# Optimization experiments

Hardware: AMD Instinct MI355X
Metric: run time of the kernel (lower is better)

## Reference

```python
import jax, jax.numpy as jnp
import numpy as np

N_NODES = 50000
EPS = 1e-12  # F.normalize eps


def sage_conv(x, src, dst, W_l, b_l, W_r):
    # PyG SAGEConv: out = lin_l(mean_j x_j) + lin_r(x_i), then L2 normalize.
    n = x.shape[0]
    agg = jax.ops.segment_sum(x[src], dst, num_segments=n)          # [N, d]
    cnt = jax.ops.segment_sum(jnp.ones_like(src, dtype=x.dtype), dst,
                              num_segments=n)                       # [N]
    mean = agg / jnp.maximum(cnt, 1.0)[:, None]
    out = mean @ W_l.T + b_l + x @ W_r.T
    norm = jnp.linalg.norm(out, axis=-1, keepdims=True)
    return out / jnp.maximum(norm, EPS)


def setup_inputs() -> dict:
    key = jax.random.key(0)
    ks = jax.random.split(key, 8)
    nfeat, nhid, nclass = 64, 64, 10
    E = 1250000
    features = jax.random.normal(ks[0], (N_NODES, nfeat), dtype=jnp.float32)
    edge_index = jax.random.randint(ks[1], (2, E), 0, N_NODES, dtype=jnp.int64)
    s1 = 1.0 / np.sqrt(nfeat)
    s2 = 1.0 / np.sqrt(nhid)
    return {
        "features": features,
        "edge_index": edge_index,
        "W1_l": jax.random.normal(ks[2], (nhid, nfeat), dtype=jnp.float32) * s1,
        "b1": jnp.zeros((nhid,), dtype=jnp.float32),
        "W1_r": jax.random.normal(ks[3], (nhid, nfeat), dtype=jnp.float32) * s1,
        "W2_l": jax.random.normal(ks[4], (nclass, nhid), dtype=jnp.float32) * s2,
        "b2": jnp.zeros((nclass,), dtype=jnp.float32),
        "W2_r": jax.random.normal(ks[5], (nclass, nhid), dtype=jnp.float32) * s2,
    }


def reference(features, edge_index, W1_l, b1, W1_r, W2_l, b2, W2_r):
    src, dst = edge_index[0], edge_index[1]
    x = jax.nn.relu(sage_conv(features, src, dst, W1_l, b1, W1_r))
    # dropout is identity in eval mode
    x = sage_conv(x, src, dst, W2_l, b2, W2_r)
    return jax.nn.log_softmax(x, axis=1)
```

## Files before the change

### kernel.cpp

```cpp
#include <hip/hip_runtime.h>
#include <hip/hip_bf16.h>


static constexpr int FEAT = 64;
static constexpr int SLOTS = 64;
static constexpr int BUCK_SZ = 6250;

__device__ __forceinline__ unsigned short f2bf(float f) {
  __hip_bfloat16 h = __float2bfloat16(f);
  return *reinterpret_cast<unsigned short*>(&h);
}
__device__ __forceinline__ unsigned int pk2(float a, float b) {
  return (unsigned)f2bf(a) | ((unsigned)f2bf(b) << 16);
}
__device__ __forceinline__ float bfl(unsigned int u) {
  return __uint_as_float(u << 16);
}
__device__ __forceinline__ float bfh(unsigned int u) {
  return __uint_as_float(u & 0xFFFF0000u);
}

__global__ __launch_bounds__(256) void fill_kernel(
    const int* __restrict__ src, const int* __restrict__ dst,
    int* __restrict__ cursor, int* __restrict__ col, int E) {
  int b = blockIdx.x & 7;
  int e = (blockIdx.x >> 3) * 256 + threadIdx.x;
  if (e >= E) return;
  int d = __builtin_nontemporal_load(dst + e);
  int lo = b * BUCK_SZ;
  if (d >= lo && d < lo + BUCK_SZ) {
    int s = __builtin_nontemporal_load(src + e);
    int pos = atomicAdd(&cursor[d], 1);
    if (pos < SLOTS) col[d * SLOTS + pos] = s;
  }
}

__global__ __launch_bounds__(256) void dense1_kernel(
    const float* __restrict__ x,
    const float* __restrict__ Wl, const float* __restrict__ Wr,
    const float* __restrict__ b,
    unsigned short* __restrict__ p, float* __restrict__ q, int N) {
  __shared__ float4 Ws[16 * 16];
  int mat = blockIdx.y >> 2;
  int og = blockIdx.y & 3;
  const float4* Wg = (const float4*)(mat ? Wr : Wl);
  int tid = threadIdx.x;
  Ws[tid] = Wg[(og * 16) * 16 + tid];
  __syncthreads();

  int node = blockIdx.x * 256 + tid;
  if (node >= N) return;

  const float4* X4 = (const float4*)x + (size_t)node * 16;
  float4 xr[16];
#pragma unroll
  for (int kq = 0; kq < 16; ++kq) xr[kq] = X4[kq];

  float acc[16];
#pragma unroll 4
  for (int o = 0; o < 16; ++o) {
    float a = 0.0f;
#pragma unroll
    for (int kq = 0; kq < 16; ++kq) {
      float4 w = Ws[o * 16 + kq];
      float4 xv = xr[kq];
      a = fmaf(xv.x, w.x, fmaf(xv.y, w.y, fmaf(xv.z, w.z, fmaf(xv.w, w.w, a))));
    }
    acc[o] = a;
  }

  if (mat) {
    float4* O4 = (float4*)(q + (size_t)node * FEAT + og * 16);
    const float4* B4 = (const float4*)(b + og * 16);
#pragma unroll
    for (int oq = 0; oq < 4; ++oq) {
      float4 bv = B4[oq];
      O4[oq] = make_float4(acc[oq * 4] + bv.x, acc[oq * 4 + 1] + bv.y,
                           acc[oq * 4 + 2] + bv.z, acc[oq * 4 + 3] + bv.w);
    }
  } else {
    uint4 w0, w1;
    w0.x = pk2(acc[0], acc[1]);
    w0.y = pk2(acc[2], acc[3]);
    w0.z = pk2(acc[4], acc[5]);
    w0.w = pk2(acc[6], acc[7]);
    w1.x = pk2(acc[8], acc[9]);
    w1.y = pk2(acc[10], acc[11]);
    w1.z = pk2(acc[12], acc[13]);
    w1.w = pk2(acc[14], acc[15]);
    uint4* O = (uint4*)p + (size_t)node * 8 + og * 2;
    O[0] = w0;
    O[1] = w1;
  }
}

__global__ __launch_bounds__(256) void gather1_kernel(
    const int* __restrict__ cursor, const int* __restrict__ col,
    const uint4* __restrict__ p1, float* __restrict__ qh, int N) {
  int tid = threadIdx.x;
  int wave = tid >> 6, lane = tid & 63;
  int g = lane >> 3, q = lane & 7;
  int node = blockIdx.x * 4 + wave;
  if (node >= N) return;

  int deg = cursor[node];
  int cnt = min(deg, SLOTS);
  int beg = node * SLOTS;
  int end = beg + cnt;

  float a[8];
#pragma unroll
  for (int j = 0; j < 8; ++j) a[j] = 0.0f;

  int e = beg + g;
  for (; e + 24 < end; e += 32) {
    int s0 = col[e], s1 = col[e + 8], s2 = col[e + 16], s3 = col[e + 24];
    uint4 w0 = p1[(size_t)s0 * 8 + q];
    uint4 w1 = p1[(size_t)s1 * 8 + q];
    uint4 w2 = p1[(size_t)s2 * 8 + q];
    uint4 w3 = p1[(size_t)s3 * 8 + q];
    a[0] += bfl(w0.x); a[1] += bfh(w0.x); a[2] += bfl(w0.y); a[3] += bfh(w0.y);
    a[4] += bfl(w0.z); a[5] += bfh(w0.z); a[6] += bfl(w0.w); a[7] += bfh(w0.w);
    a[0] += bfl(w1.x); a[1] += bfh(w1.x); a[2] += bfl(w1.y); a[3] += bfh(w1.y);
    a[4] += bfl(w1.z); a[5] += bfh(w1.z); a[6] += bfl(w1.w); a[7] += bfh(w1.w);
    a[0] += bfl(w2.x); a[1] += bfh(w2.x); a[2] += bfl(w2.y); a[3] += bfh(w2.y);
    a[4] += bfl(w2.z); a[5] += bfh(w2.z); a[6] += bfl(w2.w); a[7] += bfh(w2.w);
    a[0] += bfl(w3.x); a[1] += bfh(w3.x); a[2] += bfl(w3.y); a[3] += bfh(w3.y);
    a[4] += bfl(w3.z); a[5] += bfh(w3.z); a[6] += bfl(w3.w); a[7] += bfh(w3.w);
  }
  for (; e < end; e += 8) {
    uint4 w0 = p1[(size_t)col[e] * 8 + q];
    a[0] += bfl(w0.x); a[1] += bfh(w0.x); a[2] += bfl(w0.y); a[3] += bfh(w0.y);
    a[4] += bfl(w0.z); a[5] += bfh(w0.z); a[6] += bfl(w0.w); a[7] += bfh(w0.w);
  }

#pragma unroll
  for (int off = 8; off <= 32; off <<= 1) {
#pragma unroll
    for (int j = 0; j < 8; ++j) a[j] += __shfl_xor(a[j], off);
  }

  float invc = 1.0f / (float)max(deg, 1);
  const float4* Q4 = (const float4*)qh + (size_t)node * 16 + q * 2;
  float4 q0 = Q4[0], q1 = Q4[1];
  float v[8];
  v[0] = fmaf(a[0], invc, q0.x); v[1] = fmaf(a[1], invc, q0.y);
  v[2] = fmaf(a[2], invc, q0.z); v[3] = fmaf(a[3], invc, q0.w);
  v[4] = fmaf(a[4], invc, q1.x); v[5] = fmaf(a[5], invc, q1.y);
  v[6] = fmaf(a[6], invc, q1.z); v[7] = fmaf(a[7], invc, q1.w);

  float ss = 0.0f;
#pragma unroll
  for (int j = 0; j < 8; ++j) ss += v[j] * v[j];
#pragma unroll
  for (int off = 1; off <= 4; off <<= 1) ss += __shfl_xor(ss, off);
  float scale = 1.0f / fmaxf(sqrtf(ss), 1e-12f);

  if (g == 0) {
    float4* O4 = (float4*)qh + (size_t)node * 16 + q * 2;
    O4[0] = make_float4(fmaxf(v[0] * scale, 0.f), fmaxf(v[1] * scale, 0.f),
                        fmaxf(v[2] * scale, 0.f), fmaxf(v[3] * scale, 0.f));
    O4[1] = make_float4(fmaxf(v[4] * scale, 0.f), fmaxf(v[5] * scale, 0.f),
                        fmaxf(v[6] * scale, 0.f), fmaxf(v[7] * scale, 0.f));
  }
}

__global__ __launch_bounds__(256) void dense2_kernel(
    const float* __restrict__ h,
    const float* __restrict__ Wl, const float* __restrict__ Wr,
    const float* __restrict__ b,
    uint4* __restrict__ p2, float* __restrict__ q2, int N) {
  __shared__ float4 Wls[10 * 16];
  __shared__ float4 Wrs[10 * 16];
  __shared__ float bs[10];
  int tid = threadIdx.x;
  if (tid < 160) {
    Wls[tid] = ((const float4*)Wl)[tid];
    Wrs[tid] = ((const float4*)Wr)[tid];
  }
  if (tid < 10) bs[tid] = b[tid];
  __syncthreads();

  int node = blockIdx.x * 256 + tid;
  if (node >= N) return;

  const float4* H4 = (const float4*)h + (size_t)node * 16;
  float4 hr[16];
#pragma unroll
  for (int kq = 0; kq < 16; ++kq) hr[kq] = H4[kq];

  float pa[10], qa[10];
#pragma unroll 1
  for (int c = 0; c < 10; ++c) {
    float ap = 0.0f, aq = 0.0f;
#pragma unroll
    for (int kq = 0; kq < 16; ++kq) {
      float4 wl = Wls[c * 16 + kq];
      float4 wr = Wrs[c * 16 + kq];
      float4 hv = hr[kq];
      ap = fmaf(hv.x, wl.x, fmaf(hv.y, wl.y, fmaf(hv.z, wl.z, fmaf(hv.w, wl.w, ap))));
      aq = fmaf(hv.x, wr.x, fmaf(hv.y, wr.y, fmaf(hv.z, wr.z, fmaf(hv.w, wr.w, aq))));
    }
    pa[c] = ap;
    qa[c] = aq;
  }

  uint4 w0, w1;
  w0.x = pk2(pa[0], pa[1]); w0.y = pk2(pa[2], pa[3]);
  w0.z = pk2(pa[4], pa[5]); w0.w = pk2(pa[6], pa[7]);
  w1.x = pk2(pa[8], pa[9]); w1.y = 0u; w1.z = 0u; w1.w = 0u;
  p2[(size_t)node * 2] = w0;
  p2[(size_t)node * 2 + 1] = w1;

  float4* Q4 = (float4*)(q2 + (size_t)node * 16);
  Q4[0] = make_float4(qa[0] + bs[0], qa[1] + bs[1], qa[2] + bs[2], qa[3] + bs[3]);
  Q4[1] = make_float4(qa[4] + bs[4], qa[5] + bs[5], qa[6] + bs[6], qa[7] + bs[7]);
  Q4[2] = make_float4(qa[8] + bs[8], qa[9] + bs[9], 0.f, 0.f);
  Q4[3] = make_float4(0.f, 0.f, 0.f, 0.f);
}

__global__ __launch_bounds__(256) void gather2_kernel(
    const int* __restrict__ cursor, const int* __restrict__ col,
    const uint4* __restrict__ p2, const float* __restrict__ q2,
    float* __restrict__ out, int N) {
  int tid = threadIdx.x;
  int wave = tid >> 6, lane = tid & 63;
  int g = lane >> 1, q = lane & 1;
  int node = blockIdx.x * 4 + wave;
  if (node >= N) return;

  int deg = cursor[node];
  int cnt = min(deg, SLOTS);
  int beg = node * SLOTS;
  int end = beg + cnt;

  float a[8];
#pragma unroll
  for (int j = 0; j < 8; ++j) a[j] = 0.0f;

  int e = beg + g;
  for (; e + 32 < end; e += 64) {
    int s0 = col[e], s1 = col[e + 32];
    uint4 w0 = p2[(size_t)s0 * 2 + q];
    uint4 w1 = p2[(size_t)s1 * 2 + q];
    a[0] += bfl(w0.x); a[1] += bfh(w0.x); a[2] += bfl(w0.y); a[3] += bfh(w0.y);
    a[4] += bfl(w0.z); a[5] += bfh(w0.z); a[6] += bfl(w0.w); a[7] += bfh(w0.w);
    a[0] += bfl(w1.x); a[1] += bfh(w1.x); a[2] += bfl(w1.y); a[3] += bfh(w1.y);
    a[4] += bfl(w1.z); a[5] += bfh(w1.z); a[6] += bfl(w1.w); a[7] += bfh(w1.w);
  }
  if (e < end) {
    uint4 w0 = p2[(size_t)col[e] * 2 + q];
    a[0] += bfl(w0.x); a[1] += bfh(w0.x); a[2] += bfl(w0.y); a[3] += bfh(w0.y);
    a[4] += bfl(w0.z); a[5] += bfh(w0.z); a[6] += bfl(w0.w); a[7] += bfh(w0.w);
  }

#pragma unroll
  for (int off = 2; off <= 32; off <<= 1) {
#pragma unroll
    for (int j = 0; j < 8; ++j) a[j] += __shfl_xor(a[j], off);
  }

  float invc = 1.0f / (float)max(deg, 1);
  const float4* Q4 = (const float4*)q2 + (size_t)node * 4 + q * 2;
  float4 q0 = Q4[0], q1 = Q4[1];
  float v[8];
  v[0] = fmaf(a[0], invc, q0.x); v[1] = fmaf(a[1], invc, q0.y);
  v[2] = fmaf(a[2], invc, q0.z); v[3] = fmaf(a[3], invc, q0.w);
  v[4] = fmaf(a[4], invc, q1.x); v[5] = fmaf(a[5], invc, q1.y);
  v[6] = fmaf(a[6], invc, q1.z); v[7] = fmaf(a[7], invc, q1.w);

  float ss = 0.0f;
#pragma unroll
  for (int j = 0; j < 8; ++j) ss += v[j] * v[j];
  ss += __shfl_xor(ss, 1);
  float scale = 1.0f / fmaxf(sqrtf(ss), 1e-12f);
#pragma unroll
  for (int j = 0; j < 8; ++j) v[j] *= scale;

  float m;
  if (q == 0) {
    m = v[0];
#pragma unroll
    for (int j = 1; j < 8; ++j) m = fmaxf(m, v[j]);
  } else {
    m = fmaxf(v[0], v[1]);
  }
  m = fmaxf(m, __shfl_xor(m, 1));

  float es = 0.0f;
  if (q == 0) {
#pragma unroll
    for (int j = 0; j < 8; ++j) es += __expf(v[j] - m);
  } else {
    es = __expf(v[0] - m) + __expf(v[1] - m);
  }
  es += __shfl_xor(es, 1);
  float lse = m + __logf(es);

  if (g == 0) {
    float2* o = (float2*)(out + (size_t)node * 10);
    if (q == 0) {
      o[0] = make_float2(v[0] - lse, v[1] - lse);
      o[1] = make_float2(v[2] - lse, v[3] - lse);
      o[2] = make_float2(v[4] - lse, v[5] - lse);
      o[3] = make_float2(v[6] - lse, v[7] - lse);
    } else {
      o[4] = make_float2(v[0] - lse, v[1] - lse);
    }
  }
}

extern "C" void kernel_launch(void* const* d_in, const int* in_sizes, int n_in,
                              void* d_out, int out_size, void* d_ws, size_t ws_size,
                              hipStream_t stream) {
  const float* features = (const float*)d_in[0];
  const int* edge_index = (const int*)d_in[1];
  const float* W1_l = (const float*)d_in[2];
  const float* b1   = (const float*)d_in[3];
  const float* W1_r = (const float*)d_in[4];
  const float* W2_l = (const float*)d_in[5];
  const float* b2   = (const float*)d_in[6];
  const float* W2_r = (const float*)d_in[7];
  float* out = (float*)d_out;

  const int N = in_sizes[0] / FEAT;
  const int E = in_sizes[1] / 2;
  const int* src = edge_index;
  const int* dst = edge_index + E;

  char* ws = (char*)d_ws;
  int* cursor            = (int*)(ws + 0);
  int* col               = (int*)(ws + 200064);
  unsigned short* p1     = (unsigned short*)(ws + 13000064);
  float* q1h             = (float*)(ws + 19400064);
  uint4* p2              = (uint4*)(ws + 32200064);
  float* q2              = (float*)(ws + 33800064);

  hipMemsetAsync(cursor, 0, (size_t)N * sizeof(int), stream);

  int eb8 = ((E + 255) / 256) * 8;
  int nb256 = (N + 255) / 256;
  int nbw = (N + 3) / 4;

  fill_kernel<<<eb8, 256, 0, stream>>>(src, dst, cursor, col, E);
  dense1_kernel<<<dim3(nb256, 8), 256, 0, stream>>>(features, W1_l, W1_r, b1, p1, q1h, N);
  gather1_kernel<<<nbw, 256, 0, stream>>>(cursor, col, (const uint4*)p1, q1h, N);
  dense2_kernel<<<nb256, 256, 0, stream>>>(q1h, W2_l, W2_r, b2, p2, q2, N);
  gather2_kernel<<<nbw, 256, 0, stream>>>(cursor, col, (const uint4*)p2, q2, out, N);
}
```

Measured before the change: 226.7 us.

## Store layer-1 neighbor projections in fp8 and fold cursor reset into dense1

Layer-1 projected neighbor features are packed to fp8 instead of bf16, which halves the bytes each random gather fetches; the gather kernel is reorganized so 4 lanes cover one 64-wide row with 16 accumulators each. The memset of the degree cursor is removed and done inside dense1, which now runs before fill. Fill becomes a grid-stride kernel with a fixed block count. fp8 carries much lower precision for the aggregated mean and may hurt accuracy.

```diff
diff --git a/kernel.cpp b/kernel.cpp
--- a/kernel.cpp
+++ b/kernel.cpp
@@ -5,6 +5,9 @@
 static constexpr int FEAT = 64;
 static constexpr int SLOTS = 64;
 static constexpr int BUCK_SZ = 6250;
+static constexpr int FILL_PB = 512;
+
+typedef float v2f __attribute__((ext_vector_type(2)));
 
 __device__ __forceinline__ unsigned short f2bf(float f) {
   __hip_bfloat16 h = __float2bfloat16(f);
@@ -19,36 +22,35 @@
 __device__ __forceinline__ float bfh(unsigned int u) {
   return __uint_as_float(u & 0xFFFF0000u);
 }
-
-__global__ __launch_bounds__(256) void fill_kernel(
-    const int* __restrict__ src, const int* __restrict__ dst,
-    int* __restrict__ cursor, int* __restrict__ col, int E) {
-  int b = blockIdx.x & 7;
-  int e = (blockIdx.x >> 3) * 256 + threadIdx.x;
-  if (e >= E) return;
-  int d = __builtin_nontemporal_load(dst + e);
-  int lo = b * BUCK_SZ;
-  if (d >= lo && d < lo + BUCK_SZ) {
-    int s = __builtin_nontemporal_load(src + e);
-    int pos = atomicAdd(&cursor[d], 1);
-    if (pos < SLOTS) col[d * SLOTS + pos] = s;
-  }
+__device__ __forceinline__ void acc16(float* a, uint4 w) {
+  v2f t;
+  t = __builtin_amdgcn_cvt_pk_f32_fp8((int)w.x, false); a[0] += t.x; a[1] += t.y;
+  t = __builtin_amdgcn_cvt_pk_f32_fp8((int)w.x, true);  a[2] += t.x; a[3] += t.y;
+  t = __builtin_amdgcn_cvt_pk_f32_fp8((int)w.y, false); a[4] += t.x; a[5] += t.y;
+  t = __builtin_amdgcn_cvt_pk_f32_fp8((int)w.y, true);  a[6] += t.x; a[7] += t.y;
+  t = __builtin_amdgcn_cvt_pk_f32_fp8((int)w.z, false); a[8] += t.x; a[9] += t.y;
+  t = __builtin_amdgcn_cvt_pk_f32_fp8((int)w.z, true);  a[10] += t.x; a[11] += t.y;
+  t = __builtin_amdgcn_cvt_pk_f32_fp8((int)w.w, false); a[12] += t.x; a[13] += t.y;
+  t = __builtin_amdgcn_cvt_pk_f32_fp8((int)w.w, true);  a[14] += t.x; a[15] += t.y;
 }
 
 __global__ __launch_bounds__(256) void dense1_kernel(
     const float* __restrict__ x,
     const float* __restrict__ Wl, const float* __restrict__ Wr,
     const float* __restrict__ b,
-    unsigned short* __restrict__ p, float* __restrict__ q, int N) {
+    uint4* __restrict__ p, float* __restrict__ q,
+    int* __restrict__ cursor, int N) {
   __shared__ float4 Ws[16 * 16];
   int mat = blockIdx.y >> 2;
   int og = blockIdx.y & 3;
   const float4* Wg = (const float4*)(mat ? Wr : Wl);
   int tid = threadIdx.x;
   Ws[tid] = Wg[(og * 16) * 16 + tid];
+
+  int node = blockIdx.x * 256 + tid;
+  if (blockIdx.y == 0 && node < N) cursor[node] = 0;
   __syncthreads();
 
-  int node = blockIdx.x * 256 + tid;
   if (node >= N) return;
 
   const float4* X4 = (const float4*)x + (size_t)node * 16;
@@ -79,18 +81,38 @@
                            acc[oq * 4 + 2] + bv.z, acc[oq * 4 + 3] + bv.w);
     }
   } else {
-    uint4 w0, w1;
-    w0.x = pk2(acc[0], acc[1]);
-    w0.y = pk2(acc[2], acc[3]);
-    w0.z = pk2(acc[4], acc[5]);
-    w0.w = pk2(acc[6], acc[7]);
-    w1.x = pk2(acc[8], acc[9]);
-    w1.y = pk2(acc[10], acc[11]);
-    w1.z = pk2(acc[12], acc[13]);
-    w1.w = pk2(acc[14], acc[15]);
-    uint4* O = (uint4*)p + (size_t)node * 8 + og * 2;
-    O[0] = w0;
-    O[1] = w1;
+    unsigned int u0, u1, u2, u3;
+    u0 = __builtin_amdgcn_cvt_pk_fp8_f32(acc[0], acc[1], 0, false);
+    u0 = __builtin_amdgcn_cvt_pk_fp8_f32(acc[2], acc[3], u0, true);
+    u1 = __builtin_amdgcn_cvt_pk_fp8_f32(acc[4], acc[5], 0, false);
+    u1 = __builtin_amdgcn_cvt_pk_fp8_f32(acc[6], acc[7], u1, true);
+    u2 = __builtin_amdgcn_cvt_pk_fp8_f32(acc[8], acc[9], 0, false);
+    u2 = __builtin_amdgcn_cvt_pk_fp8_f32(acc[10], acc[11], u2, true);
+    u3 = __builtin_amdgcn_cvt_pk_fp8_f32(acc[12], acc[13], 0, false);
+    u3 = __builtin_amdgcn_cvt_pk_fp8_f32(acc[14], acc[15], u3, true);
+    uint4 w;
+    w.x = u0; w.y = u1; w.z = u2; w.w = u3;
+    p[(size_t)node * 4 + og] = w;
+  }
+}
+
+__global__ __launch_bounds__(256) void fill_kernel(
+    const int* __restrict__ src, const int* __restrict__ dst,
+    int* __restrict__ cursor, int* __restrict__ col, int E, int nchunks) {
+  int fb = blockIdx.x;
+  int bk = fb & 7;
+  int blk = fb >> 3;
+  int lo = bk * BUCK_SZ;
+  for (int chunk = blk; chunk < nchunks; chunk += FILL_PB) {
+    int e = chunk * 256 + threadIdx.x;
+    if (e < E) {
+      int d = __builtin_nontemporal_load(dst + e);
+      if (d >= lo && d < lo + BUCK_SZ) {
+        int s = __builtin_nontemporal_load(src + e);
+        int pos = atomicAdd(&cursor[d], 1);
+        if (pos < SLOTS) col[d * SLOTS + pos] = s;
+      }
+    }
   }
 }
 
@@ -99,7 +121,7 @@
     const uint4* __restrict__ p1, float* __restrict__ qh, int N) {
   int tid = threadIdx.x;
   int wave = tid >> 6, lane = tid & 63;
-  int g = lane >> 3, q = lane & 7;
+  int g = lane >> 2, q = lane & 3;
   int node = blockIdx.x * 4 + wave;
   if (node >= N) return;
 
@@ -108,60 +130,56 @@
   int beg = node * SLOTS;
   int end = beg + cnt;
 
-  float a[8];
-#pragma unroll
-  for (int j = 0; j < 8; ++j) a[j] = 0.0f;
+  float a[16];
+#pragma unroll
+  for (int j = 0; j < 16; ++j) a[j] = 0.0f;
 
   int e = beg + g;
-  for (; e + 24 < end; e += 32) {
-    int s0 = col[e], s1 = col[e + 8], s2 = col[e + 16], s3 = col[e + 24];
-    uint4 w0 = p1[(size_t)s0 * 8 + q];
-    uint4 w1 = p1[(size_t)s1 * 8 + q];
-    uint4 w2 = p1[(size_t)s2 * 8 + q];
-    uint4 w3 = p1[(size_t)s3 * 8 + q];
-    a[0] += bfl(w0.x); a[1] += bfh(w0.x); a[2] += bfl(w0.y); a[3] += bfh(w0.y);
-    a[4] += bfl(w0.z); a[5] += bfh(w0.z); a[6] += bfl(w0.w); a[7] += bfh(w0.w);
-    a[0] += bfl(w1.x); a[1] += bfh(w1.x); a[2] += bfl(w1.y); a[3] += bfh(w1.y);
-    a[4] += bfl(w1.z); a[5] += bfh(w1.z); a[6] += bfl(w1.w); a[7] += bfh(w1.w);
-    a[0] += bfl(w2.x); a[1] += bfh(w2.x); a[2] += bfl(w2.y); a[3] += bfh(w2.y);
-    a[4] += bfl(w2.z); a[5] += bfh(w2.z); a[6] += bfl(w2.w); a[7] += bfh(w2.w);
-    a[0] += bfl(w3.x); a[1] += bfh(w3.x); a[2] += bfl(w3.y); a[3] += bfh(w3.y);
-    a[4] += bfl(w3.z); a[5] += bfh(w3.z); a[6] += bfl(w3.w); a[7] += bfh(w3.w);
-  }
-  for (; e < end; e += 8) {
-    uint4 w0 = p1[(size_t)col[e] * 8 + q];
-    a[0] += bfl(w0.x); a[1] += bfh(w0.x); a[2] += bfl(w0.y); a[3] += bfh(w0.y);
-    a[4] += bfl(w0.z); a[5] += bfh(w0.z); a[6] += bfl(w0.w); a[7] += bfh(w0.w);
-  }
-
-#pragma unroll
-  for (int off = 8; off <= 32; off <<= 1) {
-#pragma unroll
-    for (int j = 0; j < 8; ++j) a[j] += __shfl_xor(a[j], off);
+  for (; e + 16 < end; e += 32) {
+    int s0 = col[e], s1 = col[e + 16];
+    uint4 w0 = p1[(size_t)s0 * 4 + q];
+    uint4 w1 = p1[(size_t)s1 * 4 + q];
+    acc16(a, w0);
+    acc16(a, w1);
+  }
+  for (; e < end; e += 16) {
+    acc16(a, p1[(size_t)col[e] * 4 + q]);
+  }
+
+#pragma unroll
+  for (int off = 4; off <= 32; off <<= 1) {
+#pragma unroll
+    for (int j = 0; j < 16; ++j) a[j] += __shfl_xor(a[j], off);
   }
 
   float invc = 1.0f / (float)max(deg, 1);
-  const float4* Q4 = (const float4*)qh + (size_t)node * 16 + q * 2;
-  float4 q0 = Q4[0], q1 = Q4[1];
-  float v[8];
-  v[0] = fmaf(a[0], invc, q0.x); v[1] = fmaf(a[1], invc, q0.y);
-  v[2] = fmaf(a[2], invc, q0.z); v[3] = fmaf(a[3], invc, q0.w);
-  v[4] = fmaf(a[4], invc, q1.x); v[5] = fmaf(a[5], invc, q1.y);
-  v[6] = fmaf(a[6], invc, q1.z); v[7] = fmaf(a[7], invc, q1.w);
+  const float4* Q4 = (const float4*)qh + (size_t)node * 16 + q * 4;
+  float v[16];
+#pragma unroll
+  for (int k = 0; k < 4; ++k) {
+    float4 qv = Q4[k];
+    v[k * 4 + 0] = fmaf(a[k * 4 + 0], invc, qv.x);
+    v[k * 4 + 1] = fmaf(a[k * 4 + 1], invc, qv.y);
+    v[k * 4 + 2] = fmaf(a[k * 4 + 2], invc, qv.z);
+    v[k * 4 + 3] = fmaf(a[k * 4 + 3], invc, qv.w);
+  }
 
   float ss = 0.0f;
 #pragma unroll
-  for (int j = 0; j < 8; ++j) ss += v[j] * v[j];
-#pragma unroll
-  for (int off = 1; off <= 4; off <<= 1) ss += __shfl_xor(ss, off);
+  for (int j = 0; j < 16; ++j) ss += v[j] * v[j];
+  ss += __shfl_xor(ss, 1);
+  ss += __shfl_xor(ss, 2);
   float scale = 1.0f / fmaxf(sqrtf(ss), 1e-12f);
 
   if (g == 0) {
-    float4* O4 = (float4*)qh + (size_t)node * 16 + q * 2;
-    O4[0] = make_float4(fmaxf(v[0] * scale, 0.f), fmaxf(v[1] * scale, 0.f),
-                        fmaxf(v[2] * scale, 0.f), fmaxf(v[3] * scale, 0.f));
-    O4[1] = make_float4(fmaxf(v[4] * scale, 0.f), fmaxf(v[5] * scale, 0.f),
-                        fmaxf(v[6] * scale, 0.f), fmaxf(v[7] * scale, 0.f));
+    float4* O4 = (float4*)qh + (size_t)node * 16 + q * 4;
+#pragma unroll
+    for (int k = 0; k < 4; ++k) {
+      O4[k] = make_float4(fmaxf(v[k * 4 + 0] * scale, 0.f),
+                          fmaxf(v[k * 4 + 1] * scale, 0.f),
+                          fmaxf(v[k * 4 + 2] * scale, 0.f),
+                          fmaxf(v[k * 4 + 3] * scale, 0.f));
+    }
   }
 }
 
@@ -331,20 +349,20 @@
   char* ws = (char*)d_ws;
   int* cursor            = (int*)(ws + 0);
   int* col               = (int*)(ws + 200064);
-  unsigned short* p1     = (unsigned short*)(ws + 13000064);
-  float* q1h             = (float*)(ws + 19400064);
-  uint4* p2              = (uint4*)(ws + 32200064);
-  float* q2              = (float*)(ws + 33800064);
-
-  hipMemsetAsync(cursor, 0, (size_t)N * sizeof(int), stream);
-
-  int eb8 = ((E + 255) / 256) * 8;
+  uint4* p1              = (uint4*)(ws + 13000064);
+  float* q1h             = (float*)(ws + 16200064);
+  uint4* p2              = (uint4*)(ws + 29000064);
+  float* q2              = (float*)(ws + 30600064);
+
+  int nchunks = (E + 255) / 256;
+  int fill_blocks = 8 * FILL_PB;
   int nb256 = (N + 255) / 256;
   int nbw = (N + 3) / 4;
 
-  fill_kernel<<<eb8, 256, 0, stream>>>(src, dst, cursor, col, E);
-  dense1_kernel<<<dim3(nb256, 8), 256, 0, stream>>>(features, W1_l, W1_r, b1, p1, q1h, N);
-  gather1_kernel<<<nbw, 256, 0, stream>>>(cursor, col, (const uint4*)p1, q1h, N);
+  dense1_kernel<<<dim3(nb256, 8), 256, 0, stream>>>(
+      features, W1_l, W1_r, b1, p1, q1h, cursor, N);
+  fill_kernel<<<fill_blocks, 256, 0, stream>>>(src, dst, cursor, col, E, nchunks);
+  gather1_kernel<<<nbw, 256, 0, stream>>>(cursor, col, p1, q1h, N);
   dense2_kernel<<<nb256, 256, 0, stream>>>(q1h, W2_l, W2_r, b2, p2, q2, N);
-  gather2_kernel<<<nbw, 256, 0, stream>>>(cursor, col, (const uint4*)p2, q2, out, N);
-}
+  gather2_kernel<<<nbw, 256, 0, stream>>>(cursor, col, p2, q2, out, N);
+}
```

Result: slower. 233.6 us (+3.1%).

## Replace bucketed CSR fill with 8-way replicated per-node slot lists

Applied to the files above, without the earlier changes.

The fill kernel no longer launches 8x blocks that each filter by destination bucket. It now does one pass, spreading atomics across 8 replicated cursor/slot arrays chosen by block index, which cuts atomic contention and redundant dst reads. Column indices shrink to 16-bit, and cursor zeroing is folded into dense1 so the memset goes away. The gathers read the 8 replicas per node and sum degrees with shuffles. Risks: unsigned short indices only hold node ids below 65536, and per-replica caps of 16 could drop edges for skewed degrees.

```diff
diff --git a/kernel.cpp b/kernel.cpp
--- a/kernel.cpp
+++ b/kernel.cpp
@@ -3,8 +3,8 @@
 
 
 static constexpr int FEAT = 64;
-static constexpr int SLOTS = 64;
-static constexpr int BUCK_SZ = 6250;
+static constexpr int NREP = 8;
+static constexpr int RSLOT = 16;
 
 __device__ __forceinline__ unsigned short f2bf(float f) {
   __hip_bfloat16 h = __float2bfloat16(f);
@@ -18,37 +18,24 @@
 }
 __device__ __forceinline__ float bfh(unsigned int u) {
   return __uint_as_float(u & 0xFFFF0000u);
-}
-
-__global__ __launch_bounds__(256) void fill_kernel(
-    const int* __restrict__ src, const int* __restrict__ dst,
-    int* __restrict__ cursor, int* __restrict__ col, int E) {
-  int b = blockIdx.x & 7;
-  int e = (blockIdx.x >> 3) * 256 + threadIdx.x;
-  if (e >= E) return;
-  int d = __builtin_nontemporal_load(dst + e);
-  int lo = b * BUCK_SZ;
-  if (d >= lo && d < lo + BUCK_SZ) {
-    int s = __builtin_nontemporal_load(src + e);
-    int pos = atomicAdd(&cursor[d], 1);
-    if (pos < SLOTS) col[d * SLOTS + pos] = s;
-  }
 }
 
 __global__ __launch_bounds__(256) void dense1_kernel(
     const float* __restrict__ x,
     const float* __restrict__ Wl, const float* __restrict__ Wr,
     const float* __restrict__ b,
-    unsigned short* __restrict__ p, float* __restrict__ q, int N) {
+    unsigned short* __restrict__ p, float* __restrict__ q,
+    int* __restrict__ cursor, int N) {
   __shared__ float4 Ws[16 * 16];
   int mat = blockIdx.y >> 2;
   int og = blockIdx.y & 3;
   const float4* Wg = (const float4*)(mat ? Wr : Wl);
   int tid = threadIdx.x;
   Ws[tid] = Wg[(og * 16) * 16 + tid];
+
+  int node = blockIdx.x * 256 + tid;
+  if (node < N) cursor[blockIdx.y * N + node] = 0;
   __syncthreads();
-
-  int node = blockIdx.x * 256 + tid;
   if (node >= N) return;
 
   const float4* X4 = (const float4*)x + (size_t)node * 16;
@@ -94,8 +81,20 @@
   }
 }
 
+__global__ __launch_bounds__(256) void fill_kernel(
+    const int* __restrict__ src, const int* __restrict__ dst,
+    int* __restrict__ cursor, unsigned short* __restrict__ col, int E, int N) {
+  int e = blockIdx.x * 256 + threadIdx.x;
+  if (e >= E) return;
+  int r = blockIdx.x & 7;
+  int d = __builtin_nontemporal_load(dst + e);
+  int s = __builtin_nontemporal_load(src + e);
+  int pos = atomicAdd(&cursor[r * N + d], 1);
+  if (pos < RSLOT) col[(size_t)(r * N + d) * RSLOT + pos] = (unsigned short)s;
+}
+
 __global__ __launch_bounds__(256) void gather1_kernel(
-    const int* __restrict__ cursor, const int* __restrict__ col,
+    const int* __restrict__ cursor, const unsigned short* __restrict__ col,
     const uint4* __restrict__ p1, float* __restrict__ qh, int N) {
   int tid = threadIdx.x;
   int wave = tid >> 6, lane = tid & 63;
@@ -103,33 +102,30 @@
   int node = blockIdx.x * 4 + wave;
   if (node >= N) return;
 
-  int deg = cursor[node];
-  int cnt = min(deg, SLOTS);
-  int beg = node * SLOTS;
-  int end = beg + cnt;
+  int cnt_raw = cursor[g * N + node];
+  int deg = cnt_raw;
+#pragma unroll
+  for (int off = 8; off <= 32; off <<= 1) deg += __shfl_xor(deg, off);
+
+  int cnt = min(cnt_raw, RSLOT);
+  const unsigned short* cbase = col + (size_t)(g * N + node) * RSLOT;
 
   float a[8];
 #pragma unroll
   for (int j = 0; j < 8; ++j) a[j] = 0.0f;
 
-  int e = beg + g;
-  for (; e + 24 < end; e += 32) {
-    int s0 = col[e], s1 = col[e + 8], s2 = col[e + 16], s3 = col[e + 24];
+  int s = 0;
+  for (; s + 1 < cnt; s += 2) {
+    int s0 = cbase[s], s1 = cbase[s + 1];
     uint4 w0 = p1[(size_t)s0 * 8 + q];
     uint4 w1 = p1[(size_t)s1 * 8 + q];
-    uint4 w2 = p1[(size_t)s2 * 8 + q];
-    uint4 w3 = p1[(size_t)s3 * 8 + q];
     a[0] += bfl(w0.x); a[1] += bfh(w0.x); a[2] += bfl(w0.y); a[3] += bfh(w0.y);
     a[4] += bfl(w0.z); a[5] += bfh(w0.z); a[6] += bfl(w0.w); a[7] += bfh(w0.w);
     a[0] += bfl(w1.x); a[1] += bfh(w1.x); a[2] += bfl(w1.y); a[3] += bfh(w1.y);
     a[4] += bfl(w1.z); a[5] += bfh(w1.z); a[6] += bfl(w1.w); a[7] += bfh(w1.w);
-    a[0] += bfl(w2.x); a[1] += bfh(w2.x); a[2] += bfl(w2.y); a[3] += bfh(w2.y);
-    a[4] += bfl(w2.z); a[5] += bfh(w2.z); a[6] += bfl(w2.w); a[7] += bfh(w2.w);
-    a[0] += bfl(w3.x); a[1] += bfh(w3.x); a[2] += bfl(w3.y); a[3] += bfh(w3.y);
-    a[4] += bfl(w3.z); a[5] += bfh(w3.z); a[6] += bfl(w3.w); a[7] += bfh(w3.w);
-  }
-  for (; e < end; e += 8) {
-    uint4 w0 = p1[(size_t)col[e] * 8 + q];
+  }
+  if (s < cnt) {
+    uint4 w0 = p1[(size_t)cbase[s] * 8 + q];
     a[0] += bfl(w0.x); a[1] += bfh(w0.x); a[2] += bfl(w0.y); a[3] += bfh(w0.y);
     a[4] += bfl(w0.z); a[5] += bfh(w0.z); a[6] += bfl(w0.w); a[7] += bfh(w0.w);
   }
@@ -220,44 +216,39 @@
 }
 
 __global__ __launch_bounds__(256) void gather2_kernel(
-    const int* __restrict__ cursor, const int* __restrict__ col,
+    const int* __restrict__ cursor, const unsigned short* __restrict__ col,
     const uint4* __restrict__ p2, const float* __restrict__ q2,
     float* __restrict__ out, int N) {
   int tid = threadIdx.x;
   int wave = tid >> 6, lane = tid & 63;
-  int g = lane >> 1, q = lane & 1;
+  int q = lane & 1;
+  int r = (lane >> 1) & 7;
+  int j = lane >> 4;
   int node = blockIdx.x * 4 + wave;
   if (node >= N) return;
 
-  int deg = cursor[node];
-  int cnt = min(deg, SLOTS);
-  int beg = node * SLOTS;
-  int end = beg + cnt;
+  int cnt_raw = cursor[r * N + node];
+  int deg = cnt_raw;
+#pragma unroll
+  for (int off = 2; off <= 8; off <<= 1) deg += __shfl_xor(deg, off);
+
+  int cnt = min(cnt_raw, RSLOT);
+  const unsigned short* cbase = col + (size_t)(r * N + node) * RSLOT;
 
   float a[8];
 #pragma unroll
-  for (int j = 0; j < 8; ++j) a[j] = 0.0f;
-
-  int e = beg + g;
-  for (; e + 32 < end; e += 64) {
-    int s0 = col[e], s1 = col[e + 32];
-    uint4 w0 = p2[(size_t)s0 * 2 + q];
-    uint4 w1 = p2[(size_t)s1 * 2 + q];
+  for (int jj = 0; jj < 8; ++jj) a[jj] = 0.0f;
+
+  for (int s = j; s < cnt; s += 4) {
+    uint4 w0 = p2[(size_t)cbase[s] * 2 + q];
     a[0] += bfl(w0.x); a[1] += bfh(w0.x); a[2] += bfl(w0.y); a[3] += bfh(w0.y);
     a[4] += bfl(w0.z); a[5] += bfh(w0.z); a[6] += bfl(w0.w); a[7] += bfh(w0.w);
-    a[0] += bfl(w1.x); a[1] += bfh(w1.x); a[2] += bfl(w1.y); a[3] += bfh(w1.y);
-    a[4] += bfl(w1.z); a[5] += bfh(w1.z); a[6] += bfl(w1.w); a[7] += bfh(w1.w);
-  }
-  if (e < end) {
-    uint4 w0 = p2[(size_t)col[e] * 2 + q];
-    a[0] += bfl(w0.x); a[1] += bfh(w0.x); a[2] += bfl(w0.y); a[3] += bfh(w0.y);
-    a[4] += bfl(w0.z); a[5] += bfh(w0.z); a[6] += bfl(w0.w); a[7] += bfh(w0.w);
   }
 
 #pragma unroll
   for (int off = 2; off <= 32; off <<= 1) {
 #pragma unroll
-    for (int j = 0; j < 8; ++j) a[j] += __shfl_xor(a[j], off);
+    for (int jj = 0; jj < 8; ++jj) a[jj] += __shfl_xor(a[jj], off);
   }
 
   float invc = 1.0f / (float)max(deg, 1);
@@ -271,17 +262,17 @@
 
   float ss = 0.0f;
 #pragma unroll
-  for (int j = 0; j < 8; ++j) ss += v[j] * v[j];
+  for (int jj = 0; jj < 8; ++jj) ss += v[jj] * v[jj];
   ss += __shfl_xor(ss, 1);
   float scale = 1.0f / fmaxf(sqrtf(ss), 1e-12f);
 #pragma unroll
-  for (int j = 0; j < 8; ++j) v[j] *= scale;
+  for (int jj = 0; jj < 8; ++jj) v[jj] *= scale;
 
   float m;
   if (q == 0) {
     m = v[0];
 #pragma unroll
-    for (int j = 1; j < 8; ++j) m = fmaxf(m, v[j]);
+    for (int jj = 1; jj < 8; ++jj) m = fmaxf(m, v[jj]);
   } else {
     m = fmaxf(v[0], v[1]);
   }
@@ -290,14 +281,14 @@
   float es = 0.0f;
   if (q == 0) {
 #pragma unroll
-    for (int j = 0; j < 8; ++j) es += __expf(v[j] - m);
+    for (int jj = 0; jj < 8; ++jj) es += __expf(v[jj] - m);
   } else {
     es = __expf(v[0] - m) + __expf(v[1] - m);
   }
   es += __shfl_xor(es, 1);
   float lse = m + __logf(es);
 
-  if (g == 0) {
+  if (lane < 2) {
     float2* o = (float2*)(out + (size_t)node * 10);
     if (q == 0) {
       o[0] = make_float2(v[0] - lse, v[1] - lse);
@@ -330,20 +321,19 @@
 
   char* ws = (char*)d_ws;
   int* cursor            = (int*)(ws + 0);
-  int* col               = (int*)(ws + 200064);
-  unsigned short* p1     = (unsigned short*)(ws + 13000064);
-  float* q1h             = (float*)(ws + 19400064);
-  uint4* p2              = (uint4*)(ws + 32200064);
-  float* q2              = (float*)(ws + 33800064);
-
-  hipMemsetAsync(cursor, 0, (size_t)N * sizeof(int), stream);
-
-  int eb8 = ((E + 255) / 256) * 8;
+  unsigned short* col    = (unsigned short*)(ws + 1600000);
+  unsigned short* p1     = (unsigned short*)(ws + 14400000);
+  float* q1h             = (float*)(ws + 20800000);
+  uint4* p2              = (uint4*)(ws + 33600000);
+  float* q2              = (float*)(ws + 35200000);
+
+  int eb = (E + 255) / 256;
   int nb256 = (N + 255) / 256;
   int nbw = (N + 3) / 4;
 
-  fill_kernel<<<eb8, 256, 0, stream>>>(src, dst, cursor, col, E);
-  dense1_kernel<<<dim3(nb256, 8), 256, 0, stream>>>(features, W1_l, W1_r, b1, p1, q1h, N);
+  dense1_kernel<<<dim3(nb256, 8), 256, 0, stream>>>(
+      features, W1_l, W1_r, b1, p1, q1h, cursor, N);
+  fill_kernel<<<eb, 256, 0, stream>>>(src, dst, cursor, col, E, N);
   gather1_kernel<<<nbw, 256, 0, stream>>>(cursor, col, (const uint4*)p1, q1h, N);
   dense2_kernel<<<nb256, 256, 0, stream>>>(q1h, W2_l, W2_r, b2, p2, q2, N);
   gather2_kernel<<<nbw, 256, 0, stream>>>(cursor, col, (const uint4*)p2, q2, out, N);
```

Result: slower. 235.2 us (+3.8%).

## Fuse CSR fill and first dense layer into one interleaved launch

Applied to the files above, without the earlier changes.

Merges the edge-bucketing fill kernel and the first dense projection kernel into a single launch. Each group of blocks holds 25 fill units plus one dense unit, so the atomic-bound fill work and the compute-bound dense work run on the GPU at the same time. This removes one kernel launch boundary and lets the two independent stages overlap. The cost is larger register/LDS pressure per block, since the fused kernel is sized for the dense path, and divergent block roles.

```diff
diff --git a/kernel.cpp b/kernel.cpp
--- a/kernel.cpp
+++ b/kernel.cpp
@@ -5,6 +5,7 @@
 static constexpr int FEAT = 64;
 static constexpr int SLOTS = 64;
 static constexpr int BUCK_SZ = 6250;
+static constexpr int ILV = 26;
 
 __device__ __forceinline__ unsigned short f2bf(float f) {
   __hip_bfloat16 h = __float2bfloat16(f);
@@ -20,35 +21,46 @@
   return __uint_as_float(u & 0xFFFF0000u);
 }
 
-__global__ __launch_bounds__(256) void fill_kernel(
-    const int* __restrict__ src, const int* __restrict__ dst,
-    int* __restrict__ cursor, int* __restrict__ col, int E) {
-  int b = blockIdx.x & 7;
-  int e = (blockIdx.x >> 3) * 256 + threadIdx.x;
-  if (e >= E) return;
-  int d = __builtin_nontemporal_load(dst + e);
-  int lo = b * BUCK_SZ;
-  if (d >= lo && d < lo + BUCK_SZ) {
-    int s = __builtin_nontemporal_load(src + e);
-    int pos = atomicAdd(&cursor[d], 1);
-    if (pos < SLOTS) col[d * SLOTS + pos] = s;
-  }
-}
-
-__global__ __launch_bounds__(256) void dense1_kernel(
+__global__ __launch_bounds__(256) void dense1_fill_kernel(
     const float* __restrict__ x,
     const float* __restrict__ Wl, const float* __restrict__ Wr,
     const float* __restrict__ b,
-    unsigned short* __restrict__ p, float* __restrict__ q, int N) {
+    unsigned short* __restrict__ p, float* __restrict__ q, int N,
+    const int* __restrict__ src, const int* __restrict__ dst,
+    int* __restrict__ cursor, int* __restrict__ col, int E,
+    int fill_units, int dense_units, int nbx) {
   __shared__ float4 Ws[16 * 16];
-  int mat = blockIdx.y >> 2;
-  int og = blockIdx.y & 3;
+  int tid = threadIdx.x;
+  int group = (int)blockIdx.x / ILV;
+  int rem = (int)blockIdx.x % ILV;
+
+  if (rem < 25) {
+    int u = group * 25 + rem;
+    if (u >= fill_units) return;
+    int bk = u & 7;
+    int e = (u >> 3) * 256 + tid;
+    if (e >= E) return;
+    int d = __builtin_nontemporal_load(dst + e);
+    int lo = bk * BUCK_SZ;
+    if (d >= lo && d < lo + BUCK_SZ) {
+      int s = __builtin_nontemporal_load(src + e);
+      int pos = atomicAdd(&cursor[d], 1);
+      if (pos < SLOTS) col[d * SLOTS + pos] = s;
+    }
+    return;
+  }
+
+  int v = group;
+  if (v >= dense_units) return;
+  int bx = v % nbx;
+  int by = v / nbx;
+  int mat = by >> 2;
+  int og = by & 3;
   const float4* Wg = (const float4*)(mat ? Wr : Wl);
-  int tid = threadIdx.x;
   Ws[tid] = Wg[(og * 16) * 16 + tid];
   __syncthreads();
 
-  int node = blockIdx.x * 256 + tid;
+  int node = bx * 256 + tid;
   if (node >= N) return;
 
   const float4* X4 = (const float4*)x + (size_t)node * 16;
@@ -338,12 +350,16 @@
 
   hipMemsetAsync(cursor, 0, (size_t)N * sizeof(int), stream);
 
-  int eb8 = ((E + 255) / 256) * 8;
+  int fill_units = ((E + 255) / 256) * 8;
   int nb256 = (N + 255) / 256;
+  int dense_units = nb256 * 8;
+  int groups = max((fill_units + 24) / 25, dense_units);
+  int grid = groups * ILV;
   int nbw = (N + 3) / 4;
 
-  fill_kernel<<<eb8, 256, 0, stream>>>(src, dst, cursor, col, E);
-  dense1_kernel<<<dim3(nb256, 8), 256, 0, stream>>>(features, W1_l, W1_r, b1, p1, q1h, N);
+  dense1_fill_kernel<<<grid, 256, 0, stream>>>(
+      features, W1_l, W1_r, b1, p1, q1h, N,
+      src, dst, cursor, col, E, fill_units, dense_units, nb256);
   gather1_kernel<<<nbw, 256, 0, stream>>>(cursor, col, (const uint4*)p1, q1h, N);
   dense2_kernel<<<nb256, 256, 0, stream>>>(q1h, W2_l, W2_r, b2, p2, q2, N);
   gather2_kernel<<<nbw, 256, 0, stream>>>(cursor, col, (const uint4*)p2, q2, out, N);
```

After: 292.2 us. 1.29x slower.
